# Performance work log

Hardware: AMD Instinct MI355X
Metric: run time of the kernel (lower is better)

The kernel has to match this reference:

```python
import jax, jax.numpy as jnp
import numpy as np
from jax import lax

TAU = 0.1
DT = 0.001
UNITS = 1024
B, T = 16, 2048


def setup_inputs() -> dict:
    key = jax.random.key(0)
    inputs = jax.random.normal(key, (B, T, UNITS), dtype=jnp.float32)
    level_var = jnp.zeros((1, UNITS), dtype=jnp.float32)
    e = np.exp(-DT / TAU)
    smoothing_init = np.log(e / (1.0 - e)).astype(np.float32)
    smoothing_var = jnp.ones((1, UNITS), dtype=jnp.float32) * smoothing_init
    return {"inputs": inputs, "level_var": level_var, "smoothing_var": smoothing_var}


def reference(inputs, level_var, smoothing_var):
    # inputs: [B, T, U]; level_var, smoothing_var: [1, U]
    s = jax.nn.sigmoid(smoothing_var)  # [1, U]
    level0 = jnp.broadcast_to(level_var, (inputs.shape[0], inputs.shape[2]))  # [B, U]

    def step(level, x_t):
        new = (1.0 - s) * x_t + s * level  # [B, U]
        return new, new

    _, levels = lax.scan(step, level0, jnp.swapaxes(inputs, 0, 1))  # [T, B, U]
    return jnp.swapaxes(levels, 0, 1)  # [B, T, U]
```

## Files before the change

### kernel.cpp

```cpp
#include <hip/hip_runtime.h>


typedef float f32x4 __attribute__((ext_vector_type(4)));

constexpr int B   = 16;
constexpr int T   = 2048;
constexpr int U   = 1024;
constexpr int U4  = U / 4;
constexpr int BU4 = B * U4;
constexpr int FLAG_STRIDE = 32;

__device__ __forceinline__ float sigmoidf(float x) {
    return 1.0f / (1.0f + __expf(-x));
}

__global__ __launch_bounds__(256, 2) void lowpass_fused(
    const f32x4* __restrict__ in,
    const float* __restrict__ level0,
    const float* __restrict__ smooth,
    float*       __restrict__ Pf,
    unsigned*    __restrict__ mask,
    f32x4*       __restrict__ out)
{
    constexpr int C  = 32;
    constexpr int L  = T / C;
    constexpr int DA = 16;
    constexpr int DB = 8;
    constexpr int LOG2L = 6;

    const int c   = (int)blockIdx.x >> 4;
    const int b   = (int)blockIdx.x & 15;
    const int tid = (int)threadIdx.x;
    const int lg  = b * U4 + tid;
    unsigned* const flag = &mask[b * FLAG_STRIDE];

    const f32x4 sm = reinterpret_cast<const f32x4*>(smooth)[tid];
    const float s0 = sigmoidf(sm.x), s1 = sigmoidf(sm.y),
                s2 = sigmoidf(sm.z), s3 = sigmoidf(sm.w);
    const float o0 = 1.0f - s0, o1 = 1.0f - s1,
                o2 = 1.0f - s2, o3 = 1.0f - s3;

    const int base = (b * T + c * L) * U4 + tid;
    const f32x4* __restrict__ ip = in + base;

    float a0 = 0.0f, a1 = 0.0f, a2 = 0.0f, a3 = 0.0f;
    {
        f32x4 buf[DA];
        #pragma unroll
        for (int i = 0; i < DA; ++i) buf[i] = ip[i * U4];

        int t = 0;
        for (; t < L - DA; t += DA) {
            #pragma unroll
            for (int j = 0; j < DA; ++j) {
                f32x4 x = buf[j];
                buf[j] = ip[(t + DA + j) * U4];
                a0 = fmaf(s0, a0, o0 * x.x);
                a1 = fmaf(s1, a1, o1 * x.y);
                a2 = fmaf(s2, a2, o2 * x.z);
                a3 = fmaf(s3, a3, o3 * x.w);
            }
        }
        #pragma unroll
        for (int j = 0; j < DA; ++j) {
            f32x4 x = buf[j];
            a0 = fmaf(s0, a0, o0 * x.x);
            a1 = fmaf(s1, a1, o1 * x.y);
            a2 = fmaf(s2, a2, o2 * x.z);
            a3 = fmaf(s3, a3, o3 * x.w);
        }
    }
    {
        const size_t po = ((size_t)c * BU4 + lg) * 4;
        __hip_atomic_store(&Pf[po + 0], a0, __ATOMIC_RELAXED, __HIP_MEMORY_SCOPE_AGENT);
        __hip_atomic_store(&Pf[po + 1], a1, __ATOMIC_RELAXED, __HIP_MEMORY_SCOPE_AGENT);
        __hip_atomic_store(&Pf[po + 2], a2, __ATOMIC_RELAXED, __HIP_MEMORY_SCOPE_AGENT);
        __hip_atomic_store(&Pf[po + 3], a3, __ATOMIC_RELAXED, __HIP_MEMORY_SCOPE_AGENT);
    }

    __syncthreads();
    if (tid == 0) {
        __hip_atomic_fetch_or(flag, 1u << c,
                              __ATOMIC_RELAXED, __HIP_MEMORY_SCOPE_AGENT);
        const unsigned need = (c == 0) ? 0u : ((1u << c) - 1u);
        if (need) {
            while ((__hip_atomic_load(flag, __ATOMIC_RELAXED,
                                      __HIP_MEMORY_SCOPE_AGENT) & need) != need) {
                __builtin_amdgcn_s_sleep(32);
            }
        }
    }
    __syncthreads();

    float sL0 = s0, sL1 = s1, sL2 = s2, sL3 = s3;
    #pragma unroll
    for (int i = 0; i < LOG2L; ++i) {
        sL0 *= sL0; sL1 *= sL1; sL2 *= sL2; sL3 *= sL3;
    }
    const f32x4 l0 = reinterpret_cast<const f32x4*>(level0)[tid];
    float v0 = l0.x, v1 = l0.y, v2 = l0.z, v3 = l0.w;
    for (int i = 0; i < c; ++i) {
        const size_t po = ((size_t)i * BU4 + lg) * 4;
        float px = __hip_atomic_load(&Pf[po + 0], __ATOMIC_RELAXED, __HIP_MEMORY_SCOPE_AGENT);
        float py = __hip_atomic_load(&Pf[po + 1], __ATOMIC_RELAXED, __HIP_MEMORY_SCOPE_AGENT);
        float pz = __hip_atomic_load(&Pf[po + 2], __ATOMIC_RELAXED, __HIP_MEMORY_SCOPE_AGENT);
        float pw = __hip_atomic_load(&Pf[po + 3], __ATOMIC_RELAXED, __HIP_MEMORY_SCOPE_AGENT);
        v0 = fmaf(sL0, v0, px);
        v1 = fmaf(sL1, v1, py);
        v2 = fmaf(sL2, v2, pz);
        v3 = fmaf(sL3, v3, pw);
    }

    f32x4* __restrict__ op = out + base;
    f32x4 buf[DB];
    #pragma unroll
    for (int i = 0; i < DB; ++i) buf[i] = ip[i * U4];

    int t = 0;
    for (; t < L - DB; t += DB) {
        #pragma unroll
        for (int j = 0; j < DB; ++j) {
            f32x4 x = buf[j];
            buf[j] = ip[(t + DB + j) * U4];
            v0 = fmaf(s0, v0, o0 * x.x);
            v1 = fmaf(s1, v1, o1 * x.y);
            v2 = fmaf(s2, v2, o2 * x.z);
            v3 = fmaf(s3, v3, o3 * x.w);
            f32x4 r; r.x = v0; r.y = v1; r.z = v2; r.w = v3;
            __builtin_nontemporal_store(r, &op[(t + j) * U4]);
        }
    }
    #pragma unroll
    for (int j = 0; j < DB; ++j) {
        f32x4 x = buf[j];
        v0 = fmaf(s0, v0, o0 * x.x);
        v1 = fmaf(s1, v1, o1 * x.y);
        v2 = fmaf(s2, v2, o2 * x.z);
        v3 = fmaf(s3, v3, o3 * x.w);
        f32x4 r; r.x = v0; r.y = v1; r.z = v2; r.w = v3;
        __builtin_nontemporal_store(r, &op[(t + j) * U4]);
    }
}

template <int C>
__global__ __launch_bounds__(256, 2) void lowpass_partial(
    const f32x4* __restrict__ in, const float* __restrict__ smooth,
    f32x4* __restrict__ P)
{
    constexpr int L  = T / C;
    constexpr int DA = 16;
    const int c   = (int)blockIdx.x >> 4;
    const int b   = (int)blockIdx.x & 15;
    const int tid = (int)threadIdx.x;
    const int lg  = b * U4 + tid;

    const f32x4 sm = reinterpret_cast<const f32x4*>(smooth)[tid];
    const float s0 = sigmoidf(sm.x), s1 = sigmoidf(sm.y),
                s2 = sigmoidf(sm.z), s3 = sigmoidf(sm.w);
    const float o0 = 1.0f - s0, o1 = 1.0f - s1,
                o2 = 1.0f - s2, o3 = 1.0f - s3;

    const f32x4* __restrict__ ip = in + (b * T + c * L) * U4 + tid;
    float a0 = 0, a1 = 0, a2 = 0, a3 = 0;
    f32x4 buf[DA];
    #pragma unroll
    for (int i = 0; i < DA; ++i) buf[i] = ip[i * U4];
    int t = 0;
    for (; t < L - DA; t += DA) {
        #pragma unroll
        for (int j = 0; j < DA; ++j) {
            f32x4 x = buf[j];
            buf[j] = ip[(t + DA + j) * U4];
            a0 = fmaf(s0, a0, o0 * x.x); a1 = fmaf(s1, a1, o1 * x.y);
            a2 = fmaf(s2, a2, o2 * x.z); a3 = fmaf(s3, a3, o3 * x.w);
        }
    }
    #pragma unroll
    for (int j = 0; j < DA; ++j) {
        f32x4 x = buf[j];
        a0 = fmaf(s0, a0, o0 * x.x); a1 = fmaf(s1, a1, o1 * x.y);
        a2 = fmaf(s2, a2, o2 * x.z); a3 = fmaf(s3, a3, o3 * x.w);
    }
    f32x4 part; part.x = a0; part.y = a1; part.z = a2; part.w = a3;
    P[c * BU4 + lg] = part;
}

template <int C>
__global__ __launch_bounds__(256, 2) void lowpass_scan(
    const f32x4* __restrict__ in, const float* __restrict__ level0,
    const float* __restrict__ smooth, const f32x4* __restrict__ P,
    f32x4* __restrict__ out)
{
    constexpr int L  = T / C;
    constexpr int DB = 8;
    constexpr int LOG2L = 31 - __builtin_clz(L);
    const int c   = (int)blockIdx.x >> 4;
    const int b   = (int)blockIdx.x & 15;
    const int tid = (int)threadIdx.x;
    const int lg  = b * U4 + tid;

    const f32x4 sm = reinterpret_cast<const f32x4*>(smooth)[tid];
    const float s0 = sigmoidf(sm.x), s1 = sigmoidf(sm.y),
                s2 = sigmoidf(sm.z), s3 = sigmoidf(sm.w);
    const float o0 = 1.0f - s0, o1 = 1.0f - s1,
                o2 = 1.0f - s2, o3 = 1.0f - s3;

    float sL0 = s0, sL1 = s1, sL2 = s2, sL3 = s3;
    #pragma unroll
    for (int i = 0; i < LOG2L; ++i) { sL0*=sL0; sL1*=sL1; sL2*=sL2; sL3*=sL3; }

    const f32x4 l0 = reinterpret_cast<const f32x4*>(level0)[tid];
    float v0 = l0.x, v1 = l0.y, v2 = l0.z, v3 = l0.w;
    for (int i = 0; i < c; ++i) {
        f32x4 p = P[i * BU4 + lg];
        v0 = fmaf(sL0, v0, p.x); v1 = fmaf(sL1, v1, p.y);
        v2 = fmaf(sL2, v2, p.z); v3 = fmaf(sL3, v3, p.w);
    }

    const int base = (b * T + c * L) * U4 + tid;
    const f32x4* __restrict__ ip = in + base;
    f32x4* __restrict__ op = out + base;
    f32x4 buf[DB];
    #pragma unroll
    for (int i = 0; i < DB; ++i) buf[i] = ip[i * U4];
    int t = 0;
    for (; t < L - DB; t += DB) {
        #pragma unroll
        for (int j = 0; j < DB; ++j) {
            f32x4 x = buf[j];
            buf[j] = ip[(t + DB + j) * U4];
            v0 = fmaf(s0, v0, o0 * x.x); v1 = fmaf(s1, v1, o1 * x.y);
            v2 = fmaf(s2, v2, o2 * x.z); v3 = fmaf(s3, v3, o3 * x.w);
            f32x4 r; r.x = v0; r.y = v1; r.z = v2; r.w = v3;
            __builtin_nontemporal_store(r, &op[(t + j) * U4]);
        }
    }
    #pragma unroll
    for (int j = 0; j < DB; ++j) {
        f32x4 x = buf[j];
        v0 = fmaf(s0, v0, o0 * x.x); v1 = fmaf(s1, v1, o1 * x.y);
        v2 = fmaf(s2, v2, o2 * x.z); v3 = fmaf(s3, v3, o3 * x.w);
        f32x4 r; r.x = v0; r.y = v1; r.z = v2; r.w = v3;
        __builtin_nontemporal_store(r, &op[(t + j) * U4]);
    }
}

extern "C" void kernel_launch(void* const* d_in, const int* in_sizes, int n_in,
                              void* d_out, int out_size, void* d_ws, size_t ws_size,
                              hipStream_t stream) {
    const f32x4* in     = (const f32x4*)d_in[0];
    const float* level0 = (const float*)d_in[1];
    const float* smooth = (const float*)d_in[2];
    f32x4* out          = (f32x4*)d_out;

    const size_t pBytes = (size_t)32 * BU4 * sizeof(f32x4);
    const size_t fBytes = (size_t)B * FLAG_STRIDE * sizeof(unsigned);

    if (ws_size >= pBytes + fBytes) {
        float* Pf      = (float*)d_ws;
        unsigned* mask = (unsigned*)((char*)d_ws + pBytes);
        (void)hipMemsetAsync(mask, 0, fBytes, stream);
        hipLaunchKernelGGL(lowpass_fused, dim3(32 * B), dim3(256), 0, stream,
                           in, level0, smooth, Pf, mask, out);
    } else {
        constexpr int C = 8;
        f32x4* P = (f32x4*)d_ws;
        dim3 grid(C * B);
        hipLaunchKernelGGL(lowpass_partial<C>, grid, dim3(256), 0, stream,
                           in, smooth, P);
        hipLaunchKernelGGL(lowpass_scan<C>,    grid, dim3(256), 0, stream,
                           in, level0, smooth, P, out);
    }
}
```

Measured before the change: 254.2 us.

## Raise time-chunk count to 64 with 64-bit mask and packed partial stores

Templates the fused chunked-scan kernel on the chunk count and launches 64 chunks per batch (1024 blocks) when the workspace allows, falling back to 32. Completion flags become 64-bit masks, and chunk partials are written and read as two 64-bit atomics instead of four 32-bit ones. Launch bounds rise to four blocks per CU. The aim is more parallelism and occupancy on a memory-bound recurrence. The cost is a longer serial carry-in loop for late chunks, more spin-waiting, and a dependence on all blocks being co-resident to avoid deadlock.

```diff
diff --git a/kernel.cpp b/kernel.cpp
--- a/kernel.cpp
+++ b/kernel.cpp
@@ -8,31 +8,37 @@
 constexpr int U   = 1024;
 constexpr int U4  = U / 4;
 constexpr int BU4 = B * U4;
-constexpr int FLAG_STRIDE = 32;
+constexpr int FLAG_STRIDE_ULL = 16;
+
+union f2u { float f[2]; unsigned long long u; };
 
 __device__ __forceinline__ float sigmoidf(float x) {
     return 1.0f / (1.0f + __expf(-x));
 }
 
-__global__ __launch_bounds__(256, 2) void lowpass_fused(
+template <int C>
+__global__ __launch_bounds__(256, 4) void lowpass_fused(
     const f32x4* __restrict__ in,
     const float* __restrict__ level0,
     const float* __restrict__ smooth,
-    float*       __restrict__ Pf,
-    unsigned*    __restrict__ mask,
+    unsigned long long* __restrict__ Pq,
+    unsigned long long* __restrict__ mask,
     f32x4*       __restrict__ out)
 {
-    constexpr int C  = 32;
     constexpr int L  = T / C;
     constexpr int DA = 16;
     constexpr int DB = 8;
-    constexpr int LOG2L = 6;
+    constexpr int LOG2L = 31 - __builtin_clz(L);
+    static_assert(L > DA && L % DA == 0, "A prefetch");
+    static_assert(L > DB && L % DB == 0, "B prefetch");
+    static_assert((1 << LOG2L) == L, "pow2");
+    static_assert(C <= 64, "mask fits u64");
 
     const int c   = (int)blockIdx.x >> 4;
     const int b   = (int)blockIdx.x & 15;
     const int tid = (int)threadIdx.x;
     const int lg  = b * U4 + tid;
-    unsigned* const flag = &mask[b * FLAG_STRIDE];
+    unsigned long long* const flag = &mask[b * FLAG_STRIDE_ULL];
 
     const f32x4 sm = reinterpret_cast<const f32x4*>(smooth)[tid];
     const float s0 = sigmoidf(sm.x), s1 = sigmoidf(sm.y),
@@ -71,18 +77,19 @@
         }
     }
     {
-        const size_t po = ((size_t)c * BU4 + lg) * 4;
-        __hip_atomic_store(&Pf[po + 0], a0, __ATOMIC_RELAXED, __HIP_MEMORY_SCOPE_AGENT);
-        __hip_atomic_store(&Pf[po + 1], a1, __ATOMIC_RELAXED, __HIP_MEMORY_SCOPE_AGENT);
-        __hip_atomic_store(&Pf[po + 2], a2, __ATOMIC_RELAXED, __HIP_MEMORY_SCOPE_AGENT);
-        __hip_atomic_store(&Pf[po + 3], a3, __ATOMIC_RELAXED, __HIP_MEMORY_SCOPE_AGENT);
+        f2u lo, hi;
+        lo.f[0] = a0; lo.f[1] = a1; hi.f[0] = a2; hi.f[1] = a3;
+        const size_t po = ((size_t)c * BU4 + lg) * 2;
+        __hip_atomic_store(&Pq[po + 0], lo.u, __ATOMIC_RELAXED, __HIP_MEMORY_SCOPE_AGENT);
+        __hip_atomic_store(&Pq[po + 1], hi.u, __ATOMIC_RELAXED, __HIP_MEMORY_SCOPE_AGENT);
     }
 
     __syncthreads();
     if (tid == 0) {
-        __hip_atomic_fetch_or(flag, 1u << c,
+        __hip_atomic_fetch_or(flag, 1ull << c,
                               __ATOMIC_RELAXED, __HIP_MEMORY_SCOPE_AGENT);
-        const unsigned need = (c == 0) ? 0u : ((1u << c) - 1u);
+        const unsigned long long need =
+            (c == 0) ? 0ull : ((1ull << c) - 1ull);
         if (need) {
             while ((__hip_atomic_load(flag, __ATOMIC_RELAXED,
                                       __HIP_MEMORY_SCOPE_AGENT) & need) != need) {
@@ -100,15 +107,14 @@
     const f32x4 l0 = reinterpret_cast<const f32x4*>(level0)[tid];
     float v0 = l0.x, v1 = l0.y, v2 = l0.z, v3 = l0.w;
     for (int i = 0; i < c; ++i) {
-        const size_t po = ((size_t)i * BU4 + lg) * 4;
-        float px = __hip_atomic_load(&Pf[po + 0], __ATOMIC_RELAXED, __HIP_MEMORY_SCOPE_AGENT);
-        float py = __hip_atomic_load(&Pf[po + 1], __ATOMIC_RELAXED, __HIP_MEMORY_SCOPE_AGENT);
-        float pz = __hip_atomic_load(&Pf[po + 2], __ATOMIC_RELAXED, __HIP_MEMORY_SCOPE_AGENT);
-        float pw = __hip_atomic_load(&Pf[po + 3], __ATOMIC_RELAXED, __HIP_MEMORY_SCOPE_AGENT);
-        v0 = fmaf(sL0, v0, px);
-        v1 = fmaf(sL1, v1, py);
-        v2 = fmaf(sL2, v2, pz);
-        v3 = fmaf(sL3, v3, pw);
+        const size_t po = ((size_t)i * BU4 + lg) * 2;
+        f2u lo, hi;
+        lo.u = __hip_atomic_load(&Pq[po + 0], __ATOMIC_RELAXED, __HIP_MEMORY_SCOPE_AGENT);
+        hi.u = __hip_atomic_load(&Pq[po + 1], __ATOMIC_RELAXED, __HIP_MEMORY_SCOPE_AGENT);
+        v0 = fmaf(sL0, v0, lo.f[0]);
+        v1 = fmaf(sL1, v1, lo.f[1]);
+        v2 = fmaf(sL2, v2, hi.f[0]);
+        v3 = fmaf(sL3, v3, hi.f[1]);
     }
 
     f32x4* __restrict__ op = out + base;
@@ -253,15 +259,24 @@
     const float* smooth = (const float*)d_in[2];
     f32x4* out          = (f32x4*)d_out;
 
-    const size_t pBytes = (size_t)32 * BU4 * sizeof(f32x4);
-    const size_t fBytes = (size_t)B * FLAG_STRIDE * sizeof(unsigned);
-
-    if (ws_size >= pBytes + fBytes) {
-        float* Pf      = (float*)d_ws;
-        unsigned* mask = (unsigned*)((char*)d_ws + pBytes);
+    const size_t fBytes = (size_t)B * FLAG_STRIDE_ULL * sizeof(unsigned long long);
+    const size_t p64 = (size_t)64 * BU4 * 16;
+    const size_t p32 = (size_t)32 * BU4 * 16;
+
+    if (ws_size >= p64 + fBytes) {
+        constexpr int C = 64;
+        unsigned long long* Pq   = (unsigned long long*)d_ws;
+        unsigned long long* mask = (unsigned long long*)((char*)d_ws + p64);
         (void)hipMemsetAsync(mask, 0, fBytes, stream);
-        hipLaunchKernelGGL(lowpass_fused, dim3(32 * B), dim3(256), 0, stream,
-                           in, level0, smooth, Pf, mask, out);
+        hipLaunchKernelGGL(lowpass_fused<C>, dim3(C * B), dim3(256), 0, stream,
+                           in, level0, smooth, Pq, mask, out);
+    } else if (ws_size >= p32 + fBytes) {
+        constexpr int C = 32;
+        unsigned long long* Pq   = (unsigned long long*)d_ws;
+        unsigned long long* mask = (unsigned long long*)((char*)d_ws + p32);
+        (void)hipMemsetAsync(mask, 0, fBytes, stream);
+        hipLaunchKernelGGL(lowpass_fused<C>, dim3(C * B), dim3(256), 0, stream,
+                           in, level0, smooth, Pq, mask, out);
     } else {
         constexpr int C = 8;
         f32x4* P = (f32x4*)d_ws;
```

Result: no change. 258.2 us (+1.6%).
